# Kernel tuning notes

Hardware: AMD Instinct MI355X
Metric: run time of the kernel (lower is better)

## Reference

```python
import jax, jax.numpy as jnp
import numpy as np

B, S, HID = 1, 2048, 2048
NH, NKV, HD = 32, 8, 64
N_REP = NH // NKV
SCALE = HD ** -0.5
NEG = -1e9  # large negative for causal mask (finite to stay fp16-safe-ish)


def _rope_tables(seq_len, head_dim, base=10000.0):
    inv_freq = 1.0 / (base ** (np.arange(0, head_dim, 2, dtype=np.float32) / head_dim))
    t = np.arange(seq_len, dtype=np.float32)
    freqs = np.outer(t, inv_freq)                      # [S, HD/2]
    emb = np.concatenate([freqs, freqs], axis=-1)      # [S, HD]
    return jnp.asarray(np.cos(emb))[None], jnp.asarray(np.sin(emb))[None]  # [1,S,HD]


def setup_inputs() -> dict:
    key = jax.random.key(0)
    k1, k2, k3, k4, k5 = jax.random.split(key, 5)
    hidden_states = jax.random.normal(k1, (B, S, HID), dtype=jnp.float32)
    cos, sin = _rope_tables(S, HD)
    # causal additive mask [1,1,S,S]
    causal = jnp.tril(jnp.ones((S, S), dtype=bool))
    attention_mask = jnp.where(causal, 0.0, NEG).astype(jnp.float32)[None, None]
    init = 0.02
    wq = jax.random.normal(k2, (NH * HD, HID), dtype=jnp.float32) * init
    wk = jax.random.normal(k3, (NKV * HD, HID), dtype=jnp.float32) * init
    wv = jax.random.normal(k4, (NKV * HD, HID), dtype=jnp.float32) * init
    wo = jax.random.normal(k5, (HID, NH * HD), dtype=jnp.float32) * init
    return {"hidden_states": hidden_states, "cos": cos, "sin": sin,
            "attention_mask": attention_mask, "wq": wq, "wk": wk, "wv": wv, "wo": wo}


def _rotate_half(x):
    x1, x2 = jnp.split(x, 2, axis=-1)
    return jnp.concatenate([-x2, x1], axis=-1)


def reference(hidden_states, cos, sin, attention_mask, wq, wk, wv, wo):
    b, s, _ = hidden_states.shape
    q = (hidden_states @ wq.T).reshape(b, s, NH, HD).transpose(0, 2, 1, 3)   # [b,nh,s,hd]
    k = (hidden_states @ wk.T).reshape(b, s, NKV, HD).transpose(0, 2, 1, 3)  # [b,nkv,s,hd]
    v = (hidden_states @ wv.T).reshape(b, s, NKV, HD).transpose(0, 2, 1, 3)
    c = cos[:, None]  # [b,1,s,hd]
    sn = sin[:, None]
    q = q * c + _rotate_half(q) * sn
    k = k * c + _rotate_half(k) * sn
    # GQA repeat_kv
    k = jnp.repeat(k, N_REP, axis=1)  # [b,nh,s,hd]
    v = jnp.repeat(v, N_REP, axis=1)
    scores = jnp.einsum('bhqd,bhkd->bhqk', q, k) * SCALE
    scores = scores.astype(jnp.float32) + attention_mask
    probs = jax.nn.softmax(scores, axis=-1).astype(q.dtype)  # dropout p=0 (eval)
    attn = jnp.einsum('bhqk,bhkd->bhqd', probs, v)
    attn = attn.transpose(0, 2, 1, 3).reshape(b, s, NH * HD)
    return attn @ wo.T
```

## Files before the change

kernel.cpp:

```cpp
#include <hip/hip_runtime.h>
#include <hip/hip_bf16.h>
#include <stdint.h>


#define S_LEN 2048
#define HIDDEN 2048
#define NH 32
#define NKV 8
#define HD 64
#define SCALE 0.125f

typedef __bf16 bf16x8 __attribute__((ext_vector_type(8)));
typedef float f32x4 __attribute__((ext_vector_type(4)));
typedef float f32x16 __attribute__((ext_vector_type(16)));

__device__ inline void gload16(const void* g, void* l) {
    using GP = const __attribute__((address_space(1))) uint32_t*;
    using LP = __attribute__((address_space(3))) uint32_t*;
    __builtin_amdgcn_global_load_lds((GP)g, (LP)(uint32_t)(uintptr_t)l, 16, 0, 0);
}

__device__ inline ushort bf16r(float x) {
    uint32_t u = __float_as_uint(x);
    return (ushort)((u + 0x7FFFu + ((u >> 16) & 1u)) >> 16);
}
__device__ inline void bsplit(float x, ushort& h, ushort& l) {
    uint32_t u = __float_as_uint(x);
    uint32_t hr = (u + 0x7FFFu + ((u >> 16) & 1u)) >> 16;
    float r = x - __uint_as_float(hr << 16);
    uint32_t ul = __float_as_uint(r);
    l = (ushort)((ul + 0x7FFFu + ((ul >> 16) & 1u)) >> 16);
    h = (ushort)hr;
}

__global__ __launch_bounds__(256) void split_bf16(
    const float* __restrict__ src, ushort* __restrict__ hi,
    ushort* __restrict__ lo, int n4)
{
    int i = blockIdx.x * 256 + threadIdx.x;
    if (i >= n4) return;
    float4 v = ((const float4*)src)[i];
    float x[4] = {v.x, v.y, v.z, v.w};
    ushort h[4], l[4];
#pragma unroll
    for (int j = 0; j < 4; j++) bsplit(x[j], h[j], l[j]);
    ushort4 ho = {h[0], h[1], h[2], h[3]};
    ushort4 lv = {l[0], l[1], l[2], l[3]};
    ((ushort4*)hi)[i] = ho;
    ((ushort4*)lo)[i] = lv;
}

template <int MODE>
__global__ __launch_bounds__(256) void mfma_gemm(
    const ushort* __restrict__ Ah, const ushort* __restrict__ Al,
    const ushort* __restrict__ Bh, const ushort* __restrict__ Bl,
    float* __restrict__ C0, float* __restrict__ C1, float* __restrict__ C2,
    int ldc)
{
    __shared__ ushort sAh[64 * 32], sAl[64 * 32];
    __shared__ ushort sBh[128 * 32], sBl[128 * 32];

    const int t = threadIdx.x;
    const int m0 = blockIdx.x * 64;
    const int n0 = blockIdx.y * 128;

    const int srow = t >> 2;
    const int skc = (t & 3) << 3;
    const ushort* aH = Ah + (size_t)(m0 + srow) * HIDDEN + skc;
    const ushort* aL = Al + (size_t)(m0 + srow) * HIDDEN + skc;
    const ushort* bH0 = Bh + (size_t)(n0 + srow) * HIDDEN + skc;
    const ushort* bH1 = Bh + (size_t)(n0 + 64 + srow) * HIDDEN + skc;
    const ushort* bL0 = Bl + (size_t)(n0 + srow) * HIDDEN + skc;
    const ushort* bL1 = Bl + (size_t)(n0 + 64 + srow) * HIDDEN + skc;
    ushort* dA_h = sAh + t * 8;
    ushort* dA_l = sAl + t * 8;
    ushort* dB_h0 = sBh + t * 8;
    ushort* dB_h1 = sBh + 64 * 32 + t * 8;
    ushort* dB_l0 = sBl + t * 8;
    ushort* dB_l1 = sBl + 64 * 32 + t * 8;

    const int lane = t & 63, w = t >> 6;
    const int fr = lane & 15;
    const int fk = lane >> 4;

    f32x4 acc[4][2];
#pragma unroll
    for (int i = 0; i < 4; i++)
#pragma unroll
        for (int j = 0; j < 2; j++) acc[i][j] = {0.f, 0.f, 0.f, 0.f};

    for (int k0 = 0; k0 < HIDDEN; k0 += 32) {
        __syncthreads();
        gload16(aH + k0, dA_h);
        gload16(aL + k0, dA_l);
        gload16(bH0 + k0, dB_h0);
        gload16(bH1 + k0, dB_h1);
        gload16(bL0 + k0, dB_l0);
        gload16(bL1 + k0, dB_l1);
        __syncthreads();

        bf16x8 ah[4], al[4], bh[2], bl[2];
#pragma unroll
        for (int fi = 0; fi < 4; fi++) {
            ah[fi] = *(const bf16x8*)&sAh[(fi * 16 + fr) * 32 + fk * 8];
            al[fi] = *(const bf16x8*)&sAl[(fi * 16 + fr) * 32 + fk * 8];
        }
#pragma unroll
        for (int fj = 0; fj < 2; fj++) {
            bh[fj] = *(const bf16x8*)&sBh[(w * 32 + fj * 16 + fr) * 32 + fk * 8];
            bl[fj] = *(const bf16x8*)&sBl[(w * 32 + fj * 16 + fr) * 32 + fk * 8];
        }
#pragma unroll
        for (int fi = 0; fi < 4; fi++)
#pragma unroll
            for (int fj = 0; fj < 2; fj++) {
                acc[fi][fj] = __builtin_amdgcn_mfma_f32_16x16x32_bf16(
                    ah[fi], bh[fj], acc[fi][fj], 0, 0, 0);
                acc[fi][fj] = __builtin_amdgcn_mfma_f32_16x16x32_bf16(
                    ah[fi], bl[fj], acc[fi][fj], 0, 0, 0);
                acc[fi][fj] = __builtin_amdgcn_mfma_f32_16x16x32_bf16(
                    al[fi], bh[fj], acc[fi][fj], 0, 0, 0);
            }
    }

#pragma unroll
    for (int fi = 0; fi < 4; fi++)
#pragma unroll
        for (int fj = 0; fj < 2; fj++) {
            int row0 = m0 + fi * 16 + fk * 4;
            int gcol = n0 + w * 32 + fj * 16 + fr;
            if (MODE == 0) {
                int slot = gcol >> 6, cin = gcol & 63;
                float* dst;
                if (slot < NH) dst = C0 + (size_t)slot * S_LEN * HD;
                else if (slot < NH + NKV) dst = C1 + (size_t)(slot - NH) * S_LEN * HD;
                else dst = C2 + (size_t)(slot - NH - NKV) * S_LEN * HD;
#pragma unroll
                for (int i = 0; i < 4; i++)
                    dst[(size_t)(row0 + i) * HD + cin] = acc[fi][fj][i];
            } else {
#pragma unroll
                for (int i = 0; i < 4; i++)
                    C0[(size_t)(row0 + i) * ldc + gcol] = acc[fi][fj][i];
            }
        }
}

__global__ __launch_bounds__(256) void rope_split(
    float* __restrict__ qd, const float* __restrict__ kd,
    const float* __restrict__ cosT, const float* __restrict__ sinT,
    ushort* __restrict__ khi, ushort* __restrict__ klo)
{
    int idx = blockIdx.x * 256 + threadIdx.x;
    int d = idx & 31;
    int s = (idx >> 5) & (S_LEN - 1);
    int slot = idx >> 16;
    float c = cosT[s * HD + d];
    float sn = sinT[s * HD + d];
    if (slot < NH) {
        float* base = qd + ((size_t)slot * S_LEN + s) * HD;
        float x1 = base[d], x2 = base[d + 32];
        base[d] = x1 * c - x2 * sn;
        base[d + 32] = x2 * c + x1 * sn;
    } else {
        const float* base = kd + ((size_t)(slot - NH) * S_LEN + s) * HD;
        float x1 = base[d], x2 = base[d + 32];
        float y1 = x1 * c - x2 * sn;
        float y2 = x2 * c + x1 * sn;
        int sw = (s & 7) << 3;
        size_t rb = ((size_t)(slot - NH) * S_LEN + s) * 64;
        ushort h1, l1, h2, l2;
        bsplit(y1, h1, l1);
        bsplit(y2, h2, l2);
        khi[rb + (d ^ sw)] = h1;        klo[rb + (d ^ sw)] = l1;
        khi[rb + ((d + 32) ^ sw)] = h2; klo[rb + ((d + 32) ^ sw)] = l2;
    }
}

__global__ __launch_bounds__(256) void split_vt(
    const float* __restrict__ v, ushort* __restrict__ vthi,
    ushort* __restrict__ vtlo)
{
    __shared__ float tile[64][65];
    const int b = blockIdx.x;
    const int hk = b >> 5, kt = b & 31;
    const float* src = v + ((size_t)hk * S_LEN + kt * 64) * 64;
    const int t = threadIdx.x;
    {
        int row = t >> 2, dg = (t & 3) * 16;
#pragma unroll
        for (int i = 0; i < 4; i++) {
            float4 x = *(const float4*)(src + row * 64 + dg + i * 4);
            tile[row][dg + i * 4 + 0] = x.x;
            tile[row][dg + i * 4 + 1] = x.y;
            tile[row][dg + i * 4 + 2] = x.z;
            tile[row][dg + i * 4 + 3] = x.w;
        }
    }
    __syncthreads();
    const int d = t >> 2, kg = (t & 3) * 16;
    ushort hi16[16], lo16[16];
#pragma unroll
    for (int i = 0; i < 16; i++) bsplit(tile[kg + i][d], hi16[i], lo16[i]);
    const int sw = (d & 7) << 3;
    size_t rowb = ((size_t)hk * 64 + d) * S_LEN + kt * 64;
    int base = kg ^ (sw & 48);
    int o0 = base + (sw & 8);
    int o1 = base + (8 ^ (sw & 8));
    *(ushort4*)&vthi[rowb + o0]     = *(ushort4*)&hi16[0];
    *(ushort4*)&vthi[rowb + o0 + 4] = *(ushort4*)&hi16[4];
    *(ushort4*)&vthi[rowb + o1]     = *(ushort4*)&hi16[8];
    *(ushort4*)&vthi[rowb + o1 + 4] = *(ushort4*)&hi16[12];
    *(ushort4*)&vtlo[rowb + o0]     = *(ushort4*)&lo16[0];
    *(ushort4*)&vtlo[rowb + o0 + 4] = *(ushort4*)&lo16[4];
    *(ushort4*)&vtlo[rowb + o1]     = *(ushort4*)&lo16[8];
    *(ushort4*)&vtlo[rowb + o1 + 4] = *(ushort4*)&lo16[12];
}

__global__ __launch_bounds__(256) void attn_mfma(
    const float* __restrict__ q,
    const ushort* __restrict__ khi, const ushort* __restrict__ klo,
    const ushort* __restrict__ vthi, const ushort* __restrict__ vtlo,
    float* __restrict__ o)
{
    __shared__ ushort uni[16384];
    __shared__ ushort Pl[4][32 * 72];
    __shared__ float corrw[4][32];
    __shared__ float lw[4][32];

    const int t = threadIdx.x;
    const int lane = t & 63, w = t >> 6;
    const int h = blockIdx.y, hk = h >> 2;
    const int qt = (int)gridDim.x - 1 - (int)blockIdx.x;
    const int q0 = qt * 128;
    const int l31 = lane & 31;
    const int dh = (lane >> 5) * 8;

    {
        const int row = t >> 1, dg = (t & 1) * 32;
        const float* src = q + ((size_t)h * S_LEN + q0 + row) * HD + dg;
        const int sw = (row & 7) << 3;
#pragma unroll
        for (int i = 0; i < 8; i++) {
            float4 v4 = *(const float4*)(src + i * 4);
            float xs[4] = {v4.x, v4.y, v4.z, v4.w};
            ushort h4[4], l4[4];
#pragma unroll
            for (int j = 0; j < 4; j++) bsplit(xs[j], h4[j], l4[j]);
            int idx = (row * 64 + dg + i * 4) ^ sw;
            *(ushort4*)&uni[idx] = *(ushort4*)&h4[0];
            *(ushort4*)&uni[8192 + idx] = *(ushort4*)&l4[0];
        }
    }
    __syncthreads();
    bf16x8 qh[4], ql[4];
    {
        const int qrow = w * 32 + l31;
        const int sw = (qrow & 7) << 3;
#pragma unroll
        for (int ks = 0; ks < 4; ks++) {
            int idx = (qrow * 64 + ks * 16 + dh) ^ sw;
            qh[ks] = *(const bf16x8*)&uni[idx];
            ql[ks] = *(const bf16x8*)&uni[8192 + idx];
        }
    }

    f32x16 accO0, accO1;
#pragma unroll
    for (int r = 0; r < 16; r++) { accO0[r] = 0.f; accO1[r] = 0.f; }
    float m_run = -1e30f, l_run = 0.f;

    const ushort* khi_t = khi + (size_t)hk * S_LEN * 64;
    const ushort* klo_t = klo + (size_t)hk * S_LEN * 64;
    const ushort* vth_t = vthi + (size_t)hk * 64 * S_LEN;
    const ushort* vtl_t = vtlo + (size_t)hk * 64 * S_LEN;
    ushort* Pw = &Pl[w][0];
    const int swk = (l31 & 7) << 3;
    const int qg = q0 + w * 32 + l31;
    const int d0s = t >> 3, kks = (t & 7) * 8;

    const int ntiles = 2 * qt + 2;
    for (int tile = 0; tile < ntiles; tile++) {
        const int k0 = tile * 64;
        __syncthreads();
        {
            const ushort* a = khi_t + k0 * 64;
            const ushort* b = klo_t + k0 * 64;
            gload16(a + t * 8, &uni[t * 8]);
            gload16(a + 2048 + t * 8, &uni[2048 + t * 8]);
            gload16(b + t * 8, &uni[4096 + t * 8]);
            gload16(b + 2048 + t * 8, &uni[6144 + t * 8]);
            gload16(vth_t + (size_t)d0s * S_LEN + k0 + kks, &uni[8192 + t * 8]);
            gload16(vth_t + (size_t)(d0s + 32) * S_LEN + k0 + kks, &uni[10240 + t * 8]);
            gload16(vtl_t + (size_t)d0s * S_LEN + k0 + kks, &uni[12288 + t * 8]);
            gload16(vtl_t + (size_t)(d0s + 32) * S_LEN + k0 + kks, &uni[14336 + t * 8]);
        }
        __syncthreads();

        f32x16 sc0, sc1;
#pragma unroll
        for (int r = 0; r < 16; r++) { sc0[r] = 0.f; sc1[r] = 0.f; }
#pragma unroll
        for (int ks = 0; ks < 4; ks++) {
            int off = ks * 16 + dh;
            int i0 = (l31 * 64 + off) ^ swk;
            int i1 = ((l31 + 32) * 64 + off) ^ swk;
            bf16x8 kh0 = *(const bf16x8*)&uni[i0];
            bf16x8 kl0 = *(const bf16x8*)&uni[4096 + i0];
            bf16x8 kh1 = *(const bf16x8*)&uni[i1];
            bf16x8 kl1 = *(const bf16x8*)&uni[4096 + i1];
            sc0 = __builtin_amdgcn_mfma_f32_32x32x16_bf16(kh0, qh[ks], sc0, 0, 0, 0);
            sc1 = __builtin_amdgcn_mfma_f32_32x32x16_bf16(kh1, qh[ks], sc1, 0, 0, 0);
            sc0 = __builtin_amdgcn_mfma_f32_32x32x16_bf16(kh0, ql[ks], sc0, 0, 0, 0);
            sc1 = __builtin_amdgcn_mfma_f32_32x32x16_bf16(kh1, ql[ks], sc1, 0, 0, 0);
            sc0 = __builtin_amdgcn_mfma_f32_32x32x16_bf16(kl0, qh[ks], sc0, 0, 0, 0);
            sc1 = __builtin_amdgcn_mfma_f32_32x32x16_bf16(kl1, qh[ks], sc1, 0, 0, 0);
        }

        const bool maskt = (tile >= 2 * qt);
        float mx = -1e30f;
#pragma unroll
        for (int r = 0; r < 16; r++) {
            int krow = (r & 3) + 8 * (r >> 2) + 4 * (lane >> 5);
            float v0 = sc0[r] * SCALE;
            float v1 = sc1[r] * SCALE;
            if (maskt) {
                if (k0 + krow > qg) v0 = -1e30f;
                if (k0 + 32 + krow > qg) v1 = -1e30f;
            }
            sc0[r] = v0; sc1[r] = v1;
            mx = fmaxf(mx, fmaxf(v0, v1));
        }
        mx = fmaxf(mx, __shfl_xor(mx, 32));

        float corr = 1.f;
        const bool skip = __all(mx - m_run <= 8.0f);
        if (!skip) {
            float m_new = fmaxf(m_run, mx);
            corr = __expf(m_run - m_new);
            m_run = m_new;
            if (lane < 32) corrw[w][l31] = corr;
        }
        float sum = 0.f;
#pragma unroll
        for (int r = 0; r < 16; r++) {
            float p0 = __expf(sc0[r] - m_run);
            float p1 = __expf(sc1[r] - m_run);
            sc0[r] = p0; sc1[r] = p1;
            sum += p0 + p1;
        }
        sum += __shfl_xor(sum, 32);
        l_run = l_run * corr + sum;

#pragma unroll
        for (int r = 0; r < 16; r += 2) {
            int krow = (r & 3) + 8 * (r >> 2) + 4 * (lane >> 5);
            uint32_t b0 = (uint32_t)bf16r(sc0[r]) | ((uint32_t)bf16r(sc0[r + 1]) << 16);
            uint32_t b1 = (uint32_t)bf16r(sc1[r]) | ((uint32_t)bf16r(sc1[r + 1]) << 16);
            *(uint32_t*)&Pw[l31 * 72 + krow] = b0;
            *(uint32_t*)&Pw[l31 * 72 + 32 + krow] = b1;
        }

        if (!skip) {
#pragma unroll
            for (int r = 0; r < 16; r++) {
                int qrow = (r & 3) + 8 * (r >> 2) + 4 * (lane >> 5);
                float cr = corrw[w][qrow];
                accO0[r] *= cr; accO1[r] *= cr;
            }
        }

#pragma unroll
        for (int ks = 0; ks < 4; ks++) {
            bf16x8 pa = *(const bf16x8*)&Pw[l31 * 72 + ks * 16 + dh];
            int ia = (l31 * 64 + ks * 16 + dh) ^ swk;
            int ib = ((l31 + 32) * 64 + ks * 16 + dh) ^ swk;
            bf16x8 vh0 = *(const bf16x8*)&uni[8192 + ia];
            bf16x8 vh1 = *(const bf16x8*)&uni[8192 + ib];
            bf16x8 vl0 = *(const bf16x8*)&uni[12288 + ia];
            bf16x8 vl1 = *(const bf16x8*)&uni[12288 + ib];
            accO0 = __builtin_amdgcn_mfma_f32_32x32x16_bf16(pa, vh0, accO0, 0, 0, 0);
            accO1 = __builtin_amdgcn_mfma_f32_32x32x16_bf16(pa, vh1, accO1, 0, 0, 0);
            accO0 = __builtin_amdgcn_mfma_f32_32x32x16_bf16(pa, vl0, accO0, 0, 0, 0);
            accO1 = __builtin_amdgcn_mfma_f32_32x32x16_bf16(pa, vl1, accO1, 0, 0, 0);
        }
    }

    if (lane < 32) lw[w][l31] = l_run;
#pragma unroll
    for (int r = 0; r < 16; r++) {
        int qrow = (r & 3) + 8 * (r >> 2) + 4 * (lane >> 5);
        float inv = 1.0f / lw[w][qrow];
        float* dst = o + (size_t)(q0 + w * 32 + qrow) * (NH * HD) + h * 64;
        dst[l31] = accO0[r] * inv;
        dst[32 + l31] = accO1[r] * inv;
    }
}

extern "C" void kernel_launch(void* const* d_in, const int* in_sizes, int n_in,
                              void* d_out, int out_size, void* d_ws, size_t ws_size,
                              hipStream_t stream) {
    const float* hidden = (const float*)d_in[0];
    const float* cosT   = (const float*)d_in[1];
    const float* sinT   = (const float*)d_in[2];
    const float* wq = (const float*)d_in[4];
    const float* wk = (const float*)d_in[5];
    const float* wv = (const float*)d_in[6];
    const float* wo = (const float*)d_in[7];
    float* out = (float*)d_out;

    char* wsb = (char*)d_ws;
    auto alloc = [&](size_t bytes) { char* p = wsb; wsb += (bytes + 255) & ~255ULL; return p; };
    float* q = (float*)alloc((size_t)NH * S_LEN * HD * 4);
    float* k = (float*)alloc((size_t)NKV * S_LEN * HD * 4);
    float* v = (float*)alloc((size_t)NKV * S_LEN * HD * 4);
    float* o = (float*)alloc((size_t)S_LEN * NH * HD * 4);
    ushort* hidH = (ushort*)alloc((size_t)S_LEN * HIDDEN * 2);
    ushort* hidL = (ushort*)alloc((size_t)S_LEN * HIDDEN * 2);
    ushort* WcH  = (ushort*)alloc((size_t)3072 * HIDDEN * 2);
    ushort* WcL  = (ushort*)alloc((size_t)3072 * HIDDEN * 2);
    ushort* woH  = (ushort*)alloc((size_t)HIDDEN * 2048 * 2);
    ushort* woL  = (ushort*)alloc((size_t)HIDDEN * 2048 * 2);
    ushort* oH   = (ushort*)alloc((size_t)S_LEN * 2048 * 2);
    ushort* oL   = (ushort*)alloc((size_t)S_LEN * 2048 * 2);
    ushort* khi  = hidH;
    ushort* klo  = hidH + 1048576;
    ushort* vthi = hidH + 2097152;
    ushort* vtlo = hidH + 3145728;

    dim3 blk(256);
    {
        int n4 = S_LEN * HIDDEN / 4;
        split_bf16<<<(n4 + 255) / 256, blk, 0, stream>>>(hidden, hidH, hidL, n4);
        int nq4 = NH * HD * HIDDEN / 4;
        split_bf16<<<(nq4 + 255) / 256, blk, 0, stream>>>(wq, WcH, WcL, nq4);
        int nk4 = NKV * HD * HIDDEN / 4;
        size_t off = (size_t)NH * HD * HIDDEN;
        split_bf16<<<(nk4 + 255) / 256, blk, 0, stream>>>(wk, WcH + off, WcL + off, nk4);
        size_t off2 = off + (size_t)NKV * HD * HIDDEN;
        split_bf16<<<(nk4 + 255) / 256, blk, 0, stream>>>(wv, WcH + off2, WcL + off2, nk4);
        int nw4 = HIDDEN * 2048 / 4;
        split_bf16<<<(nw4 + 255) / 256, blk, 0, stream>>>(wo, woH, woL, nw4);
    }
    mfma_gemm<0><<<dim3(S_LEN / 64, 3072 / 128), blk, 0, stream>>>(
        hidH, hidL, WcH, WcL, q, k, v, 0);
    rope_split<<<(NH + NKV) * S_LEN * 32 / 256, blk, 0, stream>>>(
        q, k, cosT, sinT, khi, klo);
    split_vt<<<NKV * (S_LEN / 64), blk, 0, stream>>>(v, vthi, vtlo);
    attn_mfma<<<dim3(S_LEN / 128, NH), blk, 0, stream>>>(
        q, khi, klo, vthi, vtlo, o);
    {
        int n4 = S_LEN * 2048 / 4;
        split_bf16<<<(n4 + 255) / 256, blk, 0, stream>>>(o, oH, oL, n4);
    }
    mfma_gemm<1><<<dim3(S_LEN / 64, 2048 / 128), blk, 0, stream>>>(
        oH, oL, woH, woL, out, nullptr, nullptr, 2048);
}
```

Baseline: 417.1 us.

## Swizzle GEMM LDS layout, remap blocks across XCDs, fuse output split into attention

Changes the GEMM's global-to-LDS load mapping so each row pair sits in a XOR-swizzled 128-byte line, which cuts LDS bank conflicts on the fragment reads. Remaps the 1D block index so consecutive tiles land on the same XCD for better L2 reuse. The attention kernel now writes its output directly as bf16 hi/lo halves, removing the fp32 intermediate and a separate split kernel launch. In exchange, the attention epilogue issues scattered 2-byte stores.

```diff
diff --git a/kernel.cpp b/kernel.cpp
--- a/kernel.cpp
+++ b/kernel.cpp
@@ -31,6 +31,12 @@
     uint32_t ul = __float_as_uint(r);
     l = (ushort)((ul + 0x7FFFu + ((ul >> 16) & 1u)) >> 16);
     h = (ushort)hr;
+}
+
+__device__ inline int swz_idx(int row, int fk) {
+    int line = row >> 1;
+    int inner = (((fk << 1) | (row & 1)) ^ (line & 7));
+    return line * 64 + inner * 8;
 }
 
 __global__ __launch_bounds__(256) void split_bf16(
@@ -55,34 +61,38 @@
     const ushort* __restrict__ Ah, const ushort* __restrict__ Al,
     const ushort* __restrict__ Bh, const ushort* __restrict__ Bl,
     float* __restrict__ C0, float* __restrict__ C1, float* __restrict__ C2,
-    int ldc)
+    int ldc, int nbx)
 {
     __shared__ ushort sAh[64 * 32], sAl[64 * 32];
     __shared__ ushort sBh[128 * 32], sBl[128 * 32];
 
     const int t = threadIdx.x;
-    const int m0 = blockIdx.x * 64;
-    const int n0 = blockIdx.y * 128;
-
-    const int srow = t >> 2;
-    const int skc = (t & 3) << 3;
-    const ushort* aH = Ah + (size_t)(m0 + srow) * HIDDEN + skc;
-    const ushort* aL = Al + (size_t)(m0 + srow) * HIDDEN + skc;
-    const ushort* bH0 = Bh + (size_t)(n0 + srow) * HIDDEN + skc;
-    const ushort* bH1 = Bh + (size_t)(n0 + 64 + srow) * HIDDEN + skc;
-    const ushort* bL0 = Bl + (size_t)(n0 + srow) * HIDDEN + skc;
-    const ushort* bL1 = Bl + (size_t)(n0 + 64 + srow) * HIDDEN + skc;
-    ushort* dA_h = sAh + t * 8;
-    ushort* dA_l = sAl + t * 8;
-    ushort* dB_h0 = sBh + t * 8;
-    ushort* dB_h1 = sBh + 64 * 32 + t * 8;
-    ushort* dB_l0 = sBl + t * 8;
-    ushort* dB_l1 = sBl + 64 * 32 + t * 8;
+    const int per = (int)gridDim.x >> 3;
+    const int id = (blockIdx.x & 7) * per + (blockIdx.x >> 3);
+    const int m0 = (id % nbx) * 64;
+    const int n0 = (id / nbx) * 128;
+
+    const int lineA = t >> 3;
+    const int uA = (t & 7) ^ (lineA & 7);
+    const int rowA = lineA * 2 + (uA & 1);
+    const int kA = (uA >> 1) * 8;
+    const ushort* aH = Ah + (size_t)(m0 + rowA) * HIDDEN + kA;
+    const ushort* aL = Al + (size_t)(m0 + rowA) * HIDDEN + kA;
+    const ushort* bH0 = Bh + (size_t)(n0 + rowA) * HIDDEN + kA;
+    const ushort* bH1 = Bh + (size_t)(n0 + 64 + rowA) * HIDDEN + kA;
+    const ushort* bL0 = Bl + (size_t)(n0 + rowA) * HIDDEN + kA;
+    const ushort* bL1 = Bl + (size_t)(n0 + 64 + rowA) * HIDDEN + kA;
 
     const int lane = t & 63, w = t >> 6;
     const int fr = lane & 15;
     const int fk = lane >> 4;
 
+    int idxA[4], idxB[2];
+#pragma unroll
+    for (int fi = 0; fi < 4; fi++) idxA[fi] = swz_idx(fi * 16 + fr, fk);
+#pragma unroll
+    for (int fj = 0; fj < 2; fj++) idxB[fj] = swz_idx(w * 32 + fj * 16 + fr, fk);
+
     f32x4 acc[4][2];
 #pragma unroll
     for (int i = 0; i < 4; i++)
@@ -91,24 +101,24 @@
 
     for (int k0 = 0; k0 < HIDDEN; k0 += 32) {
         __syncthreads();
-        gload16(aH + k0, dA_h);
-        gload16(aL + k0, dA_l);
-        gload16(bH0 + k0, dB_h0);
-        gload16(bH1 + k0, dB_h1);
-        gload16(bL0 + k0, dB_l0);
-        gload16(bL1 + k0, dB_l1);
+        gload16(aH + k0, sAh + t * 8);
+        gload16(aL + k0, sAl + t * 8);
+        gload16(bH0 + k0, sBh + t * 8);
+        gload16(bH1 + k0, sBh + 2048 + t * 8);
+        gload16(bL0 + k0, sBl + t * 8);
+        gload16(bL1 + k0, sBl + 2048 + t * 8);
         __syncthreads();
 
         bf16x8 ah[4], al[4], bh[2], bl[2];
 #pragma unroll
         for (int fi = 0; fi < 4; fi++) {
-            ah[fi] = *(const bf16x8*)&sAh[(fi * 16 + fr) * 32 + fk * 8];
-            al[fi] = *(const bf16x8*)&sAl[(fi * 16 + fr) * 32 + fk * 8];
+            ah[fi] = *(const bf16x8*)&sAh[idxA[fi]];
+            al[fi] = *(const bf16x8*)&sAl[idxA[fi]];
         }
 #pragma unroll
         for (int fj = 0; fj < 2; fj++) {
-            bh[fj] = *(const bf16x8*)&sBh[(w * 32 + fj * 16 + fr) * 32 + fk * 8];
-            bl[fj] = *(const bf16x8*)&sBl[(w * 32 + fj * 16 + fr) * 32 + fk * 8];
+            bh[fj] = *(const bf16x8*)&sBh[idxB[fj]];
+            bl[fj] = *(const bf16x8*)&sBl[idxB[fj]];
         }
 #pragma unroll
         for (int fi = 0; fi < 4; fi++)
@@ -221,7 +231,7 @@
     const float* __restrict__ q,
     const ushort* __restrict__ khi, const ushort* __restrict__ klo,
     const ushort* __restrict__ vthi, const ushort* __restrict__ vtlo,
-    float* __restrict__ o)
+    ushort* __restrict__ oH, ushort* __restrict__ oL)
 {
     __shared__ ushort uni[16384];
     __shared__ ushort Pl[4][32 * 72];
@@ -230,7 +240,7 @@
 
     const int t = threadIdx.x;
     const int lane = t & 63, w = t >> 6;
-    const int h = blockIdx.y, hk = h >> 2;
+    const int hd_ = blockIdx.y, hk = hd_ >> 2;
     const int qt = (int)gridDim.x - 1 - (int)blockIdx.x;
     const int q0 = qt * 128;
     const int l31 = lane & 31;
@@ -238,7 +248,7 @@
 
     {
         const int row = t >> 1, dg = (t & 1) * 32;
-        const float* src = q + ((size_t)h * S_LEN + q0 + row) * HD + dg;
+        const float* src = q + ((size_t)hd_ * S_LEN + q0 + row) * HD + dg;
         const int sw = (row & 7) << 3;
 #pragma unroll
         for (int i = 0; i < 8; i++) {
@@ -391,9 +401,14 @@
     for (int r = 0; r < 16; r++) {
         int qrow = (r & 3) + 8 * (r >> 2) + 4 * (lane >> 5);
         float inv = 1.0f / lw[w][qrow];
-        float* dst = o + (size_t)(q0 + w * 32 + qrow) * (NH * HD) + h * 64;
-        dst[l31] = accO0[r] * inv;
-        dst[32 + l31] = accO1[r] * inv;
+        float v0 = accO0[r] * inv;
+        float v1 = accO1[r] * inv;
+        size_t base = (size_t)(q0 + w * 32 + qrow) * (NH * HD) + hd_ * 64 + l31;
+        ushort hh, ll;
+        bsplit(v0, hh, ll);
+        oH[base] = hh; oL[base] = ll;
+        bsplit(v1, hh, ll);
+        oH[base + 32] = hh; oL[base + 32] = ll;
     }
 }
 
@@ -414,7 +429,6 @@
     float* q = (float*)alloc((size_t)NH * S_LEN * HD * 4);
     float* k = (float*)alloc((size_t)NKV * S_LEN * HD * 4);
     float* v = (float*)alloc((size_t)NKV * S_LEN * HD * 4);
-    float* o = (float*)alloc((size_t)S_LEN * NH * HD * 4);
     ushort* hidH = (ushort*)alloc((size_t)S_LEN * HIDDEN * 2);
     ushort* hidL = (ushort*)alloc((size_t)S_LEN * HIDDEN * 2);
     ushort* WcH  = (ushort*)alloc((size_t)3072 * HIDDEN * 2);
@@ -442,17 +456,13 @@
         int nw4 = HIDDEN * 2048 / 4;
         split_bf16<<<(nw4 + 255) / 256, blk, 0, stream>>>(wo, woH, woL, nw4);
     }
-    mfma_gemm<0><<<dim3(S_LEN / 64, 3072 / 128), blk, 0, stream>>>(
-        hidH, hidL, WcH, WcL, q, k, v, 0);
+    mfma_gemm<0><<<dim3(32 * 24), blk, 0, stream>>>(
+        hidH, hidL, WcH, WcL, q, k, v, 0, 32);
     rope_split<<<(NH + NKV) * S_LEN * 32 / 256, blk, 0, stream>>>(
         q, k, cosT, sinT, khi, klo);
     split_vt<<<NKV * (S_LEN / 64), blk, 0, stream>>>(v, vthi, vtlo);
     attn_mfma<<<dim3(S_LEN / 128, NH), blk, 0, stream>>>(
-        q, khi, klo, vthi, vtlo, o);
-    {
-        int n4 = S_LEN * 2048 / 4;
-        split_bf16<<<(n4 + 255) / 256, blk, 0, stream>>>(o, oH, oL, n4);
-    }
-    mfma_gemm<1><<<dim3(S_LEN / 64, 2048 / 128), blk, 0, stream>>>(
-        oH, oL, woH, woL, out, nullptr, nullptr, 2048);
-}
+        q, khi, klo, vthi, vtlo, oH, oL);
+    mfma_gemm<1><<<dim3(32 * 16), blk, 0, stream>>>(
+        oH, oL, woH, woL, out, nullptr, nullptr, 2048, 32);
+}
```

After: 405.3 us. 2.8% less time.
